# Kernel optimization log

Hardware: AMD Instinct MI355X
Metric: run time of the kernel (lower is better)

Reference implementation:

```python
import math
import jax, jax.numpy as jnp
import numpy as np

R, C, D, ORDER = 2048, 2048, 64, 3
O = ORDER + 1  # var_size


def setup_inputs() -> dict:
    key = jax.random.key(0)
    k1, k2, k3, k4, k5, k6 = jax.random.split(key, 6)
    return {
        "events": jax.random.randint(k1, (R, C), 0, 2, dtype=jnp.int32),
        "col_times": jax.random.uniform(k2, (C,), dtype=jnp.float32),
        "z_rows": jax.random.normal(k3, (O, R, D), dtype=jnp.float32),
        "z_cols": jax.random.normal(k4, (C, D), dtype=jnp.float32),
        "gamma_rows": jax.random.uniform(k5, (R,), dtype=jnp.float32),
        "gamma_cols": jax.random.uniform(k6, (C,), dtype=jnp.float32),
    }


def reference(events, col_times, z_rows, z_cols, gamma_rows, gamma_cols):
    o = z_rows.shape[0]
    facts = np.array([math.factorial(i) for i in range(o)], dtype=np.float32)
    # Taylor time-basis: coeffs[o, c] = t_c^o / o!   (replaces nested Python loops)
    coeffs = jnp.stack([col_times ** i for i in range(o)]) / facts[:, None]  # (O, C)
    # row positions at each column's time: (R, C, D)
    pos = jnp.einsum('ord,oc->rcd', z_rows, coeffs)
    diff = pos - z_cols[None, :, :]                        # (R, C, D)
    dist = jnp.sqrt(jnp.sum(diff * diff, axis=-1))         # (R, C) pairwise L2
    logit = gamma_rows[:, None] + gamma_cols[None, :] - dist
    # log p where p = 1 - E - (1-2E)*sigmoid(logit):
    #   E==1 -> log sigmoid(logit); E==0 -> log sigmoid(-logit)
    sign = jnp.where(events == 1, 1.0, -1.0).astype(logit.dtype)
    log_lik = jnp.sum(jax.nn.log_sigmoid(sign * logit))
    return -log_lik
```

## Files before the change

kernel.cpp:

```cpp
#include <hip/hip_runtime.h>
#include <hip/hip_bf16.h>
#include <math.h>

#define R_DIM 2048
#define C_DIM 2048
#define D_DIM 64
#define O_DIM 4
#define K_USED 272
#define K_TOT 288

typedef __attribute__((ext_vector_type(8))) short short8;
typedef __attribute__((ext_vector_type(4))) float floatx4;


__device__ __forceinline__ ushort f2bf(float f) {
  unsigned u = __float_as_uint(f);
  return (ushort)((u + 0x7FFFu + ((u >> 16) & 1u)) >> 16);
}

__device__ __forceinline__ void load16_lds(const void* g, void* l) {
  auto gp = reinterpret_cast<const __attribute__((address_space(1))) unsigned int*>(
      reinterpret_cast<uintptr_t>(g));
  auto lp = reinterpret_cast<__attribute__((address_space(3))) unsigned int*>(
      (unsigned int)reinterpret_cast<uintptr_t>(l));
  __builtin_amdgcn_global_load_lds(gp, lp, 16, 0, 0);
}

__global__ void prep_kernel(const float* __restrict__ col_times,
                            const float* __restrict__ z_rows,
                            const float* __restrict__ z_cols,
                            ushort* __restrict__ Ab,
                            ushort* __restrict__ Bb,
                            float* __restrict__ nzc,
                            float* __restrict__ out) {
  const int b = blockIdx.x;
  const int t = threadIdx.x;
  const int w = t >> 6;
  const int lane = t & 63;

  if (b == 0 && t == 0) out[0] = 0.0f;

  if (b < 512) {
    const int r = b * 4 + w;
    float zv[O_DIM];
#pragma unroll
    for (int o = 0; o < O_DIM; ++o) {
      zv[o] = z_rows[(size_t)(o * R_DIM + r) * D_DIM + lane];
      Ab[(size_t)r * K_TOT + o * 64 + lane] = f2bf(zv[o]);
    }
    float g00 = zv[0] * zv[0], g01 = zv[0] * zv[1], g02 = zv[0] * zv[2],
          g03 = zv[0] * zv[3], g11 = zv[1] * zv[1], g12 = zv[1] * zv[2],
          g13 = zv[1] * zv[3], g22 = zv[2] * zv[2], g23 = zv[2] * zv[3],
          g33 = zv[3] * zv[3];
#pragma unroll
    for (int off = 32; off > 0; off >>= 1) {
      g00 += __shfl_xor(g00, off); g01 += __shfl_xor(g01, off);
      g02 += __shfl_xor(g02, off); g03 += __shfl_xor(g03, off);
      g11 += __shfl_xor(g11, off); g12 += __shfl_xor(g12, off);
      g13 += __shfl_xor(g13, off); g22 += __shfl_xor(g22, off);
      g23 += __shfl_xor(g23, off); g33 += __shfl_xor(g33, off);
    }
    if (lane == 0) {
      ushort* e = Ab + (size_t)r * K_TOT + 256;
      e[0] = f2bf(g00);  e[1] = f2bf(g01);  e[2] = f2bf(g02);  e[3] = f2bf(g03);
      e[4] = f2bf(g01);  e[5] = f2bf(g11);  e[6] = f2bf(g12);  e[7] = f2bf(g13);
      e[8] = f2bf(g02);  e[9] = f2bf(g12);  e[10] = f2bf(g22); e[11] = f2bf(g23);
      e[12] = f2bf(g03); e[13] = f2bf(g13); e[14] = f2bf(g23); e[15] = f2bf(g33);
    }
    if (lane < 16) Ab[(size_t)r * K_TOT + K_USED + lane] = 0;
  } else {
    const int c = (b - 512) * 4 + w;
    const float tt = col_times[c];
    float cf[4];
    cf[0] = 1.0f; cf[1] = tt; cf[2] = tt * tt * 0.5f;
    cf[3] = tt * tt * tt * (1.0f / 6.0f);
    const float zc = z_cols[(size_t)c * D_DIM + lane];
#pragma unroll
    for (int o = 0; o < O_DIM; ++o)
      Bb[(size_t)c * K_TOT + o * 64 + lane] = f2bf(-2.0f * cf[o] * zc);
    float q = zc * zc;
#pragma unroll
    for (int off = 32; off > 0; off >>= 1) q += __shfl_xor(q, off);
    if (lane == 0) {
      nzc[c] = q;
      ushort* e = Bb + (size_t)c * K_TOT + 256;
#pragma unroll
      for (int i = 0; i < 16; ++i) e[i] = f2bf(cf[i >> 2] * cf[i & 3]);
    }
    if (lane < 16) Bb[(size_t)c * K_TOT + K_USED + lane] = 0;
  }
}

__launch_bounds__(256, 2)
__global__ void pair_kernel(const int* __restrict__ events,
                            const float* __restrict__ gamma_rows,
                            const float* __restrict__ gamma_cols,
                            const ushort* __restrict__ Ab,
                            const ushort* __restrict__ Bb,
                            const float* __restrict__ nzc,
                            float* __restrict__ out) {
  __shared__ __align__(16) ushort As[128 * 32];
  __shared__ __align__(16) ushort Bs[128 * 32];
  __shared__ float red[4];

  const int t = threadIdx.x;
  const int widx = t >> 6;
  const int lane = t & 63;
  const int m0 = blockIdx.y * 128;
  const int c0 = blockIdx.x * 128;
  const int wm = widx & 1;
  const int wn = widx >> 1;
  const int lm = lane & 15;
  const int kg = lane >> 4;

  floatx4 acc[4][4];
#pragma unroll
  for (int i = 0; i < 4; ++i)
#pragma unroll
    for (int j = 0; j < 4; ++j) acc[i][j] = (floatx4){0.f, 0.f, 0.f, 0.f};

  const int srow = t >> 2;
  const int selem = (t & 3) * 8;

  for (int kt = 0; kt < K_TOT; kt += 32) {
#pragma unroll
    for (int i = 0; i < 2; ++i) {
      const ushort* ga = Ab + (size_t)(m0 + srow + 64 * i) * K_TOT + kt + selem;
      load16_lds(ga, (char*)As + widx * 1024 + i * 4096);
      const ushort* gb = Bb + (size_t)(c0 + srow + 64 * i) * K_TOT + kt + selem;
      load16_lds(gb, (char*)Bs + widx * 1024 + i * 4096);
    }
    __syncthreads();

    short8 a[4], b[4];
#pragma unroll
    for (int mt = 0; mt < 4; ++mt)
      a[mt] = *(const short8*)(As + (wm * 64 + mt * 16 + lm) * 32 + kg * 8);
#pragma unroll
    for (int nt = 0; nt < 4; ++nt)
      b[nt] = *(const short8*)(Bs + (wn * 64 + nt * 16 + lm) * 32 + kg * 8);
#pragma unroll
    for (int mt = 0; mt < 4; ++mt)
#pragma unroll
      for (int nt = 0; nt < 4; ++nt)
        acc[mt][nt] = __builtin_amdgcn_mfma_f32_16x16x32_bf16(
            a[mt], b[nt], acc[mt][nt], 0, 0, 0);
    __syncthreads();
  }

  float lsum = 0.0f;
#pragma unroll
  for (int nt = 0; nt < 4; ++nt) {
    const int c = c0 + wn * 64 + nt * 16 + lm;
    const float gc = gamma_cols[c];
    const float nz = nzc[c];
#pragma unroll
    for (int mt = 0; mt < 4; ++mt) {
      const int rbase = m0 + wm * 64 + mt * 16 + kg * 4;
      const floatx4 v = acc[mt][nt];
#pragma unroll
      for (int j = 0; j < 4; ++j) {
        const int r = rbase + j;
        const float d2 = v[j] + nz;
        const float dist = sqrtf(fmaxf(d2, 0.0f));
        const float logit = gamma_rows[r] + gc - dist;
        const int ev = events[(size_t)r * C_DIM + c];
        const float x = (ev == 1) ? -logit : logit;
        lsum += fmaxf(x, 0.0f) + __logf(1.0f + __expf(-fabsf(x)));
      }
    }
  }
#pragma unroll
  for (int off = 32; off > 0; off >>= 1) lsum += __shfl_down(lsum, off);
  if (lane == 0) red[widx] = lsum;
  __syncthreads();
  if (t == 0) atomicAdd(out, red[0] + red[1] + red[2] + red[3]);
}

extern "C" void kernel_launch(void* const* d_in, const int* in_sizes, int n_in,
                              void* d_out, int out_size, void* d_ws, size_t ws_size,
                              hipStream_t stream) {
  const int* events = (const int*)d_in[0];
  const float* col_times = (const float*)d_in[1];
  const float* z_rows = (const float*)d_in[2];
  const float* z_cols = (const float*)d_in[3];
  const float* gamma_rows = (const float*)d_in[4];
  const float* gamma_cols = (const float*)d_in[5];
  float* out = (float*)d_out;

  ushort* Ab = (ushort*)d_ws;
  ushort* Bb = Ab + (size_t)R_DIM * K_TOT;
  float* nzc = (float*)(Bb + (size_t)C_DIM * K_TOT);

  prep_kernel<<<1024, 256, 0, stream>>>(col_times, z_rows, z_cols, Ab, Bb, nzc, out);
  dim3 grid(C_DIM / 128, R_DIM / 128);
  pair_kernel<<<grid, 256, 0, stream>>>(events, gamma_rows, gamma_cols, Ab, Bb,
                                        nzc, out);
}
```

Measured before the change: 99.12 us.

## Bit-pack events in prep kernel and shrink pair tiles to 64x64

The prep kernel now also packs the int32 events matrix into one bit per entry with wave ballots, and the pair kernel reads these bitmasks instead of scattered int32 event loads in its epilogue. The pair kernel tile drops from 128x128 to 64x64 per block, with launch bounds raised to 4 blocks, giving more blocks and higher occupancy but less operand reuse per block. The events matrix is still read once in full, now in prep, while the pair kernel's epilogue loads get much smaller and coalesce better. In exchange, A and B are reloaded more often from global memory and the prep kernel does more work.

```diff
diff --git a/kernel.cpp b/kernel.cpp
--- a/kernel.cpp
+++ b/kernel.cpp
@@ -8,6 +8,7 @@
 #define O_DIM 4
 #define K_USED 272
 #define K_TOT 288
+#define WB_WORDS (C_DIM / 64)
 
 typedef __attribute__((ext_vector_type(8))) short short8;
 typedef __attribute__((ext_vector_type(4))) float floatx4;
@@ -26,12 +27,14 @@
   __builtin_amdgcn_global_load_lds(gp, lp, 16, 0, 0);
 }
 
-__global__ void prep_kernel(const float* __restrict__ col_times,
+__global__ void prep_kernel(const int* __restrict__ events,
+                            const float* __restrict__ col_times,
                             const float* __restrict__ z_rows,
                             const float* __restrict__ z_cols,
                             ushort* __restrict__ Ab,
                             ushort* __restrict__ Bb,
                             float* __restrict__ nzc,
+                            unsigned long long* __restrict__ Wb,
                             float* __restrict__ out) {
   const int b = blockIdx.x;
   const int t = threadIdx.x;
@@ -68,7 +71,7 @@
       e[12] = f2bf(g03); e[13] = f2bf(g13); e[14] = f2bf(g23); e[15] = f2bf(g33);
     }
     if (lane < 16) Ab[(size_t)r * K_TOT + K_USED + lane] = 0;
-  } else {
+  } else if (b < 1024) {
     const int c = (b - 512) * 4 + w;
     const float tt = col_times[c];
     float cf[4];
@@ -88,84 +91,99 @@
       for (int i = 0; i < 16; ++i) e[i] = f2bf(cf[i >> 2] * cf[i & 3]);
     }
     if (lane < 16) Bb[(size_t)c * K_TOT + K_USED + lane] = 0;
-  }
-}
-
-__launch_bounds__(256, 2)
-__global__ void pair_kernel(const int* __restrict__ events,
-                            const float* __restrict__ gamma_rows,
+  } else {
+    const int r = b - 1024;
+    const int cbase = w * 512;
+#pragma unroll
+    for (int i = 0; i < 8; ++i) {
+      const int col = cbase + i * 64 + lane;
+      const int ev = events[(size_t)r * C_DIM + col];
+      const unsigned long long mask = __ballot(ev == 1);
+      if (lane == 0) Wb[r * WB_WORDS + (cbase >> 6) + i] = mask;
+    }
+  }
+}
+
+__launch_bounds__(256, 4)
+__global__ void pair_kernel(const float* __restrict__ gamma_rows,
                             const float* __restrict__ gamma_cols,
                             const ushort* __restrict__ Ab,
                             const ushort* __restrict__ Bb,
                             const float* __restrict__ nzc,
+                            const unsigned long long* __restrict__ Wb,
                             float* __restrict__ out) {
-  __shared__ __align__(16) ushort As[128 * 32];
-  __shared__ __align__(16) ushort Bs[128 * 32];
+  __shared__ __align__(16) ushort As[64 * 32];
+  __shared__ __align__(16) ushort Bs[64 * 32];
   __shared__ float red[4];
 
   const int t = threadIdx.x;
   const int widx = t >> 6;
   const int lane = t & 63;
-  const int m0 = blockIdx.y * 128;
-  const int c0 = blockIdx.x * 128;
+  const int m0 = blockIdx.y * 64;
+  const int c0 = blockIdx.x * 64;
   const int wm = widx & 1;
   const int wn = widx >> 1;
   const int lm = lane & 15;
   const int kg = lane >> 4;
 
-  floatx4 acc[4][4];
-#pragma unroll
-  for (int i = 0; i < 4; ++i)
-#pragma unroll
-    for (int j = 0; j < 4; ++j) acc[i][j] = (floatx4){0.f, 0.f, 0.f, 0.f};
+  floatx4 acc[2][2];
+#pragma unroll
+  for (int i = 0; i < 2; ++i)
+#pragma unroll
+    for (int j = 0; j < 2; ++j) acc[i][j] = (floatx4){0.f, 0.f, 0.f, 0.f};
 
   const int srow = t >> 2;
   const int selem = (t & 3) * 8;
 
   for (int kt = 0; kt < K_TOT; kt += 32) {
-#pragma unroll
-    for (int i = 0; i < 2; ++i) {
-      const ushort* ga = Ab + (size_t)(m0 + srow + 64 * i) * K_TOT + kt + selem;
-      load16_lds(ga, (char*)As + widx * 1024 + i * 4096);
-      const ushort* gb = Bb + (size_t)(c0 + srow + 64 * i) * K_TOT + kt + selem;
-      load16_lds(gb, (char*)Bs + widx * 1024 + i * 4096);
-    }
+    load16_lds(Ab + (size_t)(m0 + srow) * K_TOT + kt + selem,
+               (char*)As + widx * 1024);
+    load16_lds(Bb + (size_t)(c0 + srow) * K_TOT + kt + selem,
+               (char*)Bs + widx * 1024);
     __syncthreads();
 
-    short8 a[4], b[4];
-#pragma unroll
-    for (int mt = 0; mt < 4; ++mt)
-      a[mt] = *(const short8*)(As + (wm * 64 + mt * 16 + lm) * 32 + kg * 8);
-#pragma unroll
-    for (int nt = 0; nt < 4; ++nt)
-      b[nt] = *(const short8*)(Bs + (wn * 64 + nt * 16 + lm) * 32 + kg * 8);
-#pragma unroll
-    for (int mt = 0; mt < 4; ++mt)
-#pragma unroll
-      for (int nt = 0; nt < 4; ++nt)
+    short8 a[2], b[2];
+#pragma unroll
+    for (int mt = 0; mt < 2; ++mt)
+      a[mt] = *(const short8*)(As + (wm * 32 + mt * 16 + lm) * 32 + kg * 8);
+#pragma unroll
+    for (int nt = 0; nt < 2; ++nt)
+      b[nt] = *(const short8*)(Bs + (wn * 32 + nt * 16 + lm) * 32 + kg * 8);
+#pragma unroll
+    for (int mt = 0; mt < 2; ++mt)
+#pragma unroll
+      for (int nt = 0; nt < 2; ++nt)
         acc[mt][nt] = __builtin_amdgcn_mfma_f32_16x16x32_bf16(
             a[mt], b[nt], acc[mt][nt], 0, 0, 0);
     __syncthreads();
   }
 
+  float gc[2], nz[2];
+  int cbit[2];
+#pragma unroll
+  for (int nt = 0; nt < 2; ++nt) {
+    const int c = c0 + wn * 32 + nt * 16 + lm;
+    gc[nt] = gamma_cols[c];
+    nz[nt] = nzc[c];
+    cbit[nt] = c & 63;
+  }
+  const int wword = blockIdx.x;
   float lsum = 0.0f;
 #pragma unroll
-  for (int nt = 0; nt < 4; ++nt) {
-    const int c = c0 + wn * 64 + nt * 16 + lm;
-    const float gc = gamma_cols[c];
-    const float nz = nzc[c];
-#pragma unroll
-    for (int mt = 0; mt < 4; ++mt) {
-      const int rbase = m0 + wm * 64 + mt * 16 + kg * 4;
-      const floatx4 v = acc[mt][nt];
-#pragma unroll
-      for (int j = 0; j < 4; ++j) {
-        const int r = rbase + j;
-        const float d2 = v[j] + nz;
+  for (int mt = 0; mt < 2; ++mt) {
+    const int rbase = m0 + wm * 32 + mt * 16 + kg * 4;
+#pragma unroll
+    for (int j = 0; j < 4; ++j) {
+      const int r = rbase + j;
+      const float gr = gamma_rows[r];
+      const unsigned long long wbits = Wb[r * WB_WORDS + wword];
+#pragma unroll
+      for (int nt = 0; nt < 2; ++nt) {
+        const float d2 = acc[mt][nt][j] + nz[nt];
         const float dist = sqrtf(fmaxf(d2, 0.0f));
-        const float logit = gamma_rows[r] + gc - dist;
-        const int ev = events[(size_t)r * C_DIM + c];
-        const float x = (ev == 1) ? -logit : logit;
+        const float logit = gr + gc[nt] - dist;
+        const int ev = (int)((wbits >> cbit[nt]) & 1ull);
+        const float x = ev ? -logit : logit;
         lsum += fmaxf(x, 0.0f) + __logf(1.0f + __expf(-fabsf(x)));
       }
     }
@@ -191,9 +209,11 @@
   ushort* Ab = (ushort*)d_ws;
   ushort* Bb = Ab + (size_t)R_DIM * K_TOT;
   float* nzc = (float*)(Bb + (size_t)C_DIM * K_TOT);
-
-  prep_kernel<<<1024, 256, 0, stream>>>(col_times, z_rows, z_cols, Ab, Bb, nzc, out);
-  dim3 grid(C_DIM / 128, R_DIM / 128);
-  pair_kernel<<<grid, 256, 0, stream>>>(events, gamma_rows, gamma_cols, Ab, Bb,
-                                        nzc, out);
-}
+  unsigned long long* Wb = (unsigned long long*)(nzc + C_DIM);
+
+  prep_kernel<<<3072, 256, 0, stream>>>(events, col_times, z_rows, z_cols, Ab,
+                                        Bb, nzc, Wb, out);
+  dim3 grid(C_DIM / 64, R_DIM / 64);
+  pair_kernel<<<grid, 256, 0, stream>>>(gamma_rows, gamma_cols, Ab, Bb, nzc, Wb,
+                                        out);
+}
```

After: 95.49 us. 3.7% less time.
